# Optimization experiments

Measured on AMD Instinct MI355X. Metric: run time of the kernel, lower is better.

## Reference

```python
import jax, jax.numpy as jnp
import numpy as np

# Constant from livnium.kernel.constants (assumed scalar; value taken as 1.0).
K_O = 1.0
EPS = 1e-12  # F.normalize default eps

B, D, C = 16384, 1024, 3
F_DIM = D + 10  # features = h_final (D) + 10 scalar features


def setup_inputs() -> dict:
    key = jax.random.key(0)
    ks = jax.random.split(key, 8)
    s1 = 1.0 / np.sqrt(F_DIM)
    return {
        "h_final": jax.random.normal(ks[0], (B, D), jnp.float32),
        "v_p": jax.random.normal(ks[1], (B, D), jnp.float32),
        "v_h": jax.random.normal(ks[2], (B, D), jnp.float32),
        "neutral_dir": jax.random.normal(ks[3], (D,), jnp.float32),
        "neutral_scale": jnp.array(1.0, jnp.float32),
        "w1": jax.random.normal(ks[4], (F_DIM, F_DIM), jnp.float32) * s1,
        "b1": jnp.zeros((F_DIM,), jnp.float32),
        "w2": jax.random.normal(ks[5], (C, F_DIM), jnp.float32) * s1,
        "b2": jnp.zeros((C,), jnp.float32),
    }


def _normalize(x, axis):
    n = jnp.linalg.norm(x, axis=axis, keepdims=True)
    return x / jnp.maximum(n, EPS)


def reference(h_final, v_p, v_h, neutral_dir, neutral_scale, w1, b1, w2, b2):
    v_p_n = _normalize(v_p, -1)                      # [B, D]
    v_h_n = _normalize(v_h, -1)                      # [B, D]
    nd_n = _normalize(neutral_dir, 0)                # [D]

    # alignment(): cosine of the unit vectors == batched dot product.
    align = jnp.sum(v_p_n * v_h_n, axis=-1, keepdims=True)        # [B, 1]
    opp = jnp.sum(-v_p_n * v_h_n, axis=-1, keepdims=True)          # [B, 1]
    align_neutral_p = neutral_scale * jnp.sum(v_p_n * nd_n, axis=-1, keepdims=True)
    align_neutral_h = neutral_scale * jnp.sum(v_h_n * nd_n, axis=-1, keepdims=True)

    energy = K_O * ((1.0 + align) * 0.5)
    expose_neg = (1.0 - align) * 0.5
    dist_p_h = jnp.linalg.norm(v_h - v_p, axis=-1, keepdims=True)
    r_p = jnp.linalg.norm(v_p, axis=-1, keepdims=True)
    r_h = jnp.linalg.norm(v_h, axis=-1, keepdims=True)
    r_final = jnp.linalg.norm(h_final, axis=-1, keepdims=True)

    features = jnp.concatenate(
        [h_final, align, opp, energy, expose_neg, dist_p_h,
         r_p, r_h, r_final, align_neutral_p, align_neutral_h], axis=-1)  # [B, D+10]

    hidden = jax.nn.relu(features @ w1.T + b1)
    logits = hidden @ w2.T + b2                      # [B, C]
    return logits
```

## Files before the change

### kernel.cpp

```cpp
#include <hip/hip_runtime.h>
#include <cstdint>
#include <cstddef>

#define B_ROWS 16384
#define D_DIM  1024
#define F_REAL 1034
#define N_PAD  1152
#define K_PAD  1088
#define NKT    34
#define EPSN   1e-12f

typedef __bf16 bf16x8 __attribute__((ext_vector_type(8)));
typedef float  f32x4  __attribute__((ext_vector_type(4)));
typedef unsigned short u16;

__device__ __forceinline__ u16 f2bf(float f) {
    __bf16 b = (__bf16)f;
    return __builtin_bit_cast(u16, b);
}

__global__ __launch_bounds__(256)
void prep_kernel(const float* __restrict__ h, const float* __restrict__ vp,
                 const float* __restrict__ vh, const float* __restrict__ nd,
                 const float* __restrict__ nsp, u16* __restrict__ A)
{
    const int tid  = threadIdx.x;
    const int lane = tid & 63;
    const int wg   = blockIdx.x * 4 + (tid >> 6);
    const int r0   = wg * 4;

    const float4* ndp = (const float4*)nd;
    float4 n[4];
    #pragma unroll
    for (int c = 0; c < 4; ++c) n[c] = ndp[lane + c * 64];
    const float ns = nsp[0];

    float s_nn = 0.f;
    #pragma unroll
    for (int c = 0; c < 4; ++c)
        s_nn += n[c].x*n[c].x + n[c].y*n[c].y + n[c].z*n[c].z + n[c].w*n[c].w;
    #pragma unroll
    for (int m = 32; m >= 1; m >>= 1) s_nn += __shfl_xor(s_nn, m, 64);
    const float nnc = fmaxf(sqrtf(s_nn), EPSN);

    float4 P[2][4], Q[2][4], F[2][4];

#define LOADR(st, r)                                                          \
    do {                                                                      \
        const float4* vpp = (const float4*)(vp + (size_t)(r) * D_DIM);        \
        const float4* vhp = (const float4*)(vh + (size_t)(r) * D_DIM);        \
        const float4* hp  = (const float4*)(h  + (size_t)(r) * D_DIM);        \
        _Pragma("unroll")                                                     \
        for (int c = 0; c < 4; ++c) P[st][c] = vpp[lane + c * 64];            \
        _Pragma("unroll")                                                     \
        for (int c = 0; c < 4; ++c) Q[st][c] = vhp[lane + c * 64];            \
        _Pragma("unroll")                                                     \
        for (int c = 0; c < 4; ++c) F[st][c] = hp[lane + c * 64];             \
    } while (0)

    LOADR(0, r0);
    #pragma unroll
    for (int i = 0; i < 4; ++i) {
        const int st = i & 1;
        if (i + 1 < 4) LOADR(((i + 1) & 1), r0 + i + 1);
        __builtin_amdgcn_sched_barrier(0);

        float s_pp = 0.f, s_hh = 0.f, s_pv = 0.f, s_ff = 0.f;
        float s_dd = 0.f, s_pn = 0.f, s_hn = 0.f;
        #pragma unroll
        for (int c = 0; c < 4; ++c) {
            float4 p = P[st][c], q = Q[st][c], f = F[st][c], nn = n[c];
            s_pp += p.x*p.x + p.y*p.y + p.z*p.z + p.w*p.w;
            s_hh += q.x*q.x + q.y*q.y + q.z*q.z + q.w*q.w;
            s_pv += p.x*q.x + p.y*q.y + p.z*q.z + p.w*q.w;
            s_ff += f.x*f.x + f.y*f.y + f.z*f.z + f.w*f.w;
            float dx = q.x-p.x, dy = q.y-p.y, dz = q.z-p.z, dw = q.w-p.w;
            s_dd += dx*dx + dy*dy + dz*dz + dw*dw;
            s_pn += p.x*nn.x + p.y*nn.y + p.z*nn.z + p.w*nn.w;
            s_hn += q.x*nn.x + q.y*nn.y + q.z*nn.z + q.w*nn.w;
        }

        u16* arow = A + (size_t)(r0 + i) * K_PAD;
        #pragma unroll
        for (int c = 0; c < 4; ++c) {
            ushort4 hc;
            hc.x = f2bf(F[st][c].x); hc.y = f2bf(F[st][c].y);
            hc.z = f2bf(F[st][c].z); hc.w = f2bf(F[st][c].w);
            *(ushort4*)(arow + (lane + c * 64) * 4) = hc;
        }

        #pragma unroll
        for (int m = 32; m >= 1; m >>= 1) {
            s_pp += __shfl_xor(s_pp, m, 64);
            s_hh += __shfl_xor(s_hh, m, 64);
            s_pv += __shfl_xor(s_pv, m, 64);
            s_ff += __shfl_xor(s_ff, m, 64);
            s_dd += __shfl_xor(s_dd, m, 64);
            s_pn += __shfl_xor(s_pn, m, 64);
            s_hn += __shfl_xor(s_hn, m, 64);
        }

        if (lane == 0) {
            float np_ = sqrtf(s_pp), nh_ = sqrtf(s_hh), nf = sqrtf(s_ff);
            float npc = fmaxf(np_, EPSN), nhc = fmaxf(nh_, EPSN);
            float align = s_pv / (npc * nhc);
            u16 fo[64];
            fo[0] = f2bf(align);
            fo[1] = f2bf(-align);
            fo[2] = f2bf(0.5f * (1.0f + align));
            fo[3] = f2bf(0.5f * (1.0f - align));
            fo[4] = f2bf(sqrtf(s_dd));
            fo[5] = f2bf(np_);
            fo[6] = f2bf(nh_);
            fo[7] = f2bf(nf);
            fo[8] = f2bf(ns * s_pn / (npc * nnc));
            fo[9] = f2bf(ns * s_hn / (nhc * nnc));
            #pragma unroll
            for (int k = 10; k < 64; ++k) fo[k] = 0;
            #pragma unroll
            for (int k = 0; k < 8; ++k)
                *(uint4*)(arow + D_DIM + k * 8) = *(uint4*)(fo + k * 8);
        }
    }
#undef LOADR
}

__global__ __launch_bounds__(256)
void convw_kernel(const float* __restrict__ w1, u16* __restrict__ Bm)
{
    const int i = blockIdx.x;
    for (int j = threadIdx.x; j < K_PAD; j += 256) {
        float v = (i < F_REAL && j < F_REAL) ? w1[(size_t)i * F_REAL + j] : 0.0f;
        Bm[(size_t)i * K_PAD + j] = f2bf(v);
    }
}

__global__ __launch_bounds__(256)
void initout_kernel(const float* __restrict__ b2, float* __restrict__ out)
{
    int i = blockIdx.x * 256 + threadIdx.x;
    if (i < B_ROWS * 3) out[i] = b2[i % 3];
}

__global__ __launch_bounds__(256)
void gemm_kernel(const u16* __restrict__ A,
                 const u16* __restrict__ Bm,
                 const float* __restrict__ b1, const float* __restrict__ w2,
                 float* __restrict__ out)
{
    __shared__ __bf16 As[2 * 128 * 32];
    __shared__ __bf16 Bs[2 * 128 * 32];

    const int tid  = threadIdx.x;
    const int lane = tid & 63;
    const int wave = tid >> 6;
    const int wm = wave >> 1, wn = wave & 1;
    const int bm = blockIdx.x, bn = blockIdx.y;

    const u16* srcA[2];
    const u16* srcB[2];
    #pragma unroll
    for (int l = 0; l < 2; ++l) {
        int s   = l * 256 + tid;
        int row = s >> 2;
        int c   = (s & 3) ^ ((s >> 3) & 3);
        srcA[l] = A  + (size_t)(bm * 128 + row) * K_PAD + c * 8;
        srcB[l] = Bm + (size_t)(bn * 128 + row) * K_PAD + c * 8;
    }
    const int ldsbase = wave * 512;

#define STAGE(buf, kt)                                                        \
    do {                                                                      \
        _Pragma("unroll")                                                     \
        for (int l = 0; l < 2; ++l) {                                         \
            __builtin_amdgcn_global_load_lds(                                 \
                (const __attribute__((address_space(1))) void*)(srcA[l] + (kt) * 32), \
                (__attribute__((address_space(3))) void*)(As + (buf) * 4096 + l * 2048 + ldsbase), \
                16, 0, 0);                                                    \
            __builtin_amdgcn_global_load_lds(                                 \
                (const __attribute__((address_space(1))) void*)(srcB[l] + (kt) * 32), \
                (__attribute__((address_space(3))) void*)(Bs + (buf) * 4096 + l * 2048 + ldsbase), \
                16, 0, 0);                                                    \
        }                                                                     \
    } while (0)

    const int col  = lane & 15;
    const int quad = lane >> 4;
    const int swz  = quad ^ ((col >> 1) & 3);
    int aoff[4], boff[4];
    #pragma unroll
    for (int i = 0; i < 4; ++i)
        aoff[i] = (wm * 64 + i * 16 + col) * 32 + swz * 8;
    #pragma unroll
    for (int j = 0; j < 4; ++j)
        boff[j] = (wn * 64 + j * 16 + col) * 32 + swz * 8;

    f32x4 acc[4][4];
    #pragma unroll
    for (int i = 0; i < 4; ++i)
        #pragma unroll
        for (int j = 0; j < 4; ++j)
            acc[i][j] = (f32x4){0.f, 0.f, 0.f, 0.f};

#define COMPUTE(buf)                                                          \
    do {                                                                      \
        const __bf16* Ab = As + (buf) * 4096;                                 \
        const __bf16* Bb = Bs + (buf) * 4096;                                 \
        bf16x8 av[4], bv[4];                                                  \
        _Pragma("unroll")                                                     \
        for (int i = 0; i < 4; ++i) av[i] = *(const bf16x8*)(Ab + aoff[i]);   \
        _Pragma("unroll")                                                     \
        for (int j = 0; j < 4; ++j) bv[j] = *(const bf16x8*)(Bb + boff[j]);   \
        _Pragma("unroll")                                                     \
        for (int i = 0; i < 4; ++i)                                           \
            _Pragma("unroll")                                                 \
            for (int j = 0; j < 4; ++j)                                       \
                acc[i][j] = __builtin_amdgcn_mfma_f32_16x16x32_bf16(          \
                                av[i], bv[j], acc[i][j], 0, 0, 0);            \
    } while (0)

    STAGE(0, 0);
    __syncthreads();

    for (int kt = 0; kt < NKT; kt += 2) {
        STAGE(1, kt + 1);
        COMPUTE(0);
        __syncthreads();
        if (kt + 2 < NKT) STAGE(0, kt + 2);
        COMPUTE(1);
        __syncthreads();
    }

    float bias[4], w20[4], w21[4], w22[4];
    #pragma unroll
    for (int ni = 0; ni < 4; ++ni) {
        int n = bn * 128 + wn * 64 + ni * 16 + col;
        bool v = n < F_REAL;
        bias[ni] = v ? b1[n] : 0.0f;
        w20[ni]  = v ? w2[n] : 0.0f;
        w21[ni]  = v ? w2[F_REAL + n] : 0.0f;
        w22[ni]  = v ? w2[2 * F_REAL + n] : 0.0f;
    }
    #pragma unroll
    for (int mi = 0; mi < 4; ++mi) {
        float c0[4] = {0,0,0,0}, c1[4] = {0,0,0,0}, c2[4] = {0,0,0,0};
        #pragma unroll
        for (int ni = 0; ni < 4; ++ni) {
            #pragma unroll
            for (int r = 0; r < 4; ++r) {
                float hd = fmaxf(acc[mi][ni][r] + bias[ni], 0.0f);
                c0[r] += hd * w20[ni];
                c1[r] += hd * w21[ni];
                c2[r] += hd * w22[ni];
            }
        }
        #pragma unroll
        for (int m = 8; m >= 1; m >>= 1) {
            #pragma unroll
            for (int r = 0; r < 4; ++r) {
                c0[r] += __shfl_xor(c0[r], m, 64);
                c1[r] += __shfl_xor(c1[r], m, 64);
                c2[r] += __shfl_xor(c2[r], m, 64);
            }
        }
        if (col == 0) {
            int gm = bm * 128 + wm * 64 + mi * 16 + quad * 4;
            #pragma unroll
            for (int r = 0; r < 4; ++r) {
                atomicAdd(out + (size_t)(gm + r) * 3 + 0, c0[r]);
                atomicAdd(out + (size_t)(gm + r) * 3 + 1, c1[r]);
                atomicAdd(out + (size_t)(gm + r) * 3 + 2, c2[r]);
            }
        }
    }
#undef STAGE
#undef COMPUTE
}

extern "C" void kernel_launch(void* const* d_in, const int* in_sizes, int n_in,
                              void* d_out, int out_size, void* d_ws, size_t ws_size,
                              hipStream_t stream)
{
    const float* h  = (const float*)d_in[0];
    const float* vp = (const float*)d_in[1];
    const float* vh = (const float*)d_in[2];
    const float* nd = (const float*)d_in[3];
    const float* ns = (const float*)d_in[4];
    const float* w1 = (const float*)d_in[5];
    const float* b1 = (const float*)d_in[6];
    const float* w2 = (const float*)d_in[7];
    const float* b2 = (const float*)d_in[8];
    float* out = (float*)d_out;

    u16* Afull = (u16*)d_ws;
    u16* Bfull = Afull + (size_t)B_ROWS * K_PAD;

    prep_kernel<<<1024, 256, 0, stream>>>(h, vp, vh, nd, ns, Afull);
    convw_kernel<<<N_PAD, 256, 0, stream>>>(w1, Bfull);
    initout_kernel<<<(B_ROWS * 3 + 255) / 256, 256, 0, stream>>>(b2, out);
    gemm_kernel<<<dim3(B_ROWS / 128, N_PAD / 128), 256, 0, stream>>>(
        Afull, Bfull, b1, w2, out);
}
```

Measured before the change: 311.4 us.

## Triple-buffer GEMM K-loop with single barrier and XCD-aware block mapping

Moves the GEMM main loop from a double buffer with two barriers per iteration to a three-stage LDS ring, where each step waits only on older loads (vmcnt) and issues one barrier. The epilogue's bias and w2 loads are hoisted ahead of the loop, and MFMA sections are raised with s_setprio. The 2D grid is flattened and remapped so each XCD works on a contiguous band of row tiles across all column tiles, to improve L2 reuse of A. LDS use grows by half, and the hand-written waitcnt counts must match the loads each STAGE issues.

```diff
diff --git a/kernel.cpp b/kernel.cpp
--- a/kernel.cpp
+++ b/kernel.cpp
@@ -148,14 +148,19 @@
                  const float* __restrict__ b1, const float* __restrict__ w2,
                  float* __restrict__ out)
 {
-    __shared__ __bf16 As[2 * 128 * 32];
-    __shared__ __bf16 Bs[2 * 128 * 32];
+    __shared__ __bf16 As[3 * 128 * 32];
+    __shared__ __bf16 Bs[3 * 128 * 32];
 
     const int tid  = threadIdx.x;
     const int lane = tid & 63;
     const int wave = tid >> 6;
     const int wm = wave >> 1, wn = wave & 1;
-    const int bm = blockIdx.x, bn = blockIdx.y;
+
+    const int flat = blockIdx.x;
+    const int xcd  = flat & 7;
+    const int kk   = flat >> 3;
+    const int bm   = xcd * 16 + kk / 9;
+    const int bn   = kk % 9;
 
     const u16* srcA[2];
     const u16* srcB[2];
@@ -219,18 +224,6 @@
                                 av[i], bv[j], acc[i][j], 0, 0, 0);            \
     } while (0)
 
-    STAGE(0, 0);
-    __syncthreads();
-
-    for (int kt = 0; kt < NKT; kt += 2) {
-        STAGE(1, kt + 1);
-        COMPUTE(0);
-        __syncthreads();
-        if (kt + 2 < NKT) STAGE(0, kt + 2);
-        COMPUTE(1);
-        __syncthreads();
-    }
-
     float bias[4], w20[4], w21[4], w22[4];
     #pragma unroll
     for (int ni = 0; ni < 4; ++ni) {
@@ -241,6 +234,31 @@
         w21[ni]  = v ? w2[F_REAL + n] : 0.0f;
         w22[ni]  = v ? w2[2 * F_REAL + n] : 0.0f;
     }
+    asm volatile("s_waitcnt vmcnt(0)" ::: "memory");
+    __builtin_amdgcn_sched_barrier(0);
+
+    STAGE(0, 0);
+    STAGE(1, 1);
+
+    int cb = 0;
+    for (int t = 0; t < NKT - 1; ++t) {
+        asm volatile("s_waitcnt vmcnt(4)\n\ts_barrier" ::: "memory");
+        __builtin_amdgcn_sched_barrier(0);
+        if (t + 2 < NKT) {
+            int nb = cb + 2; if (nb >= 3) nb -= 3;
+            STAGE(nb, t + 2);
+        }
+        __builtin_amdgcn_s_setprio(1);
+        COMPUTE(cb);
+        __builtin_amdgcn_s_setprio(0);
+        if (++cb == 3) cb = 0;
+    }
+    asm volatile("s_waitcnt vmcnt(0)\n\ts_barrier" ::: "memory");
+    __builtin_amdgcn_sched_barrier(0);
+    __builtin_amdgcn_s_setprio(1);
+    COMPUTE(cb);
+    __builtin_amdgcn_s_setprio(0);
+
     #pragma unroll
     for (int mi = 0; mi < 4; ++mi) {
         float c0[4] = {0,0,0,0}, c1[4] = {0,0,0,0}, c2[4] = {0,0,0,0};
@@ -298,6 +316,6 @@
     prep_kernel<<<1024, 256, 0, stream>>>(h, vp, vh, nd, ns, Afull);
     convw_kernel<<<N_PAD, 256, 0, stream>>>(w1, Bfull);
     initout_kernel<<<(B_ROWS * 3 + 255) / 256, 256, 0, stream>>>(b2, out);
-    gemm_kernel<<<dim3(B_ROWS / 128, N_PAD / 128), 256, 0, stream>>>(
+    gemm_kernel<<<B_ROWS / 128 * (N_PAD / 128), 256, 0, stream>>>(
         Afull, Bfull, b1, w2, out);
 }
```

Result: slower. 331.7 us (+6.5%).

## Fuse h_final bf16 conversion into GEMM with LDS-resident A panel and pre-swizzled W1

Applied to the files above, without the earlier changes.

Drops the materialised bf16 A matrix. Each GEMM block of 64 rows now loads its h_final rows directly into a swizzled LDS panel, computes the row norm there, and loops over all N tiles. Each wave reads W1 straight from global memory in an MFMA fragment layout pre-arranged by convw. The scalar features go through a small side buffer. The cross-block atomics and the init kernel are replaced by an in-block reduction and a direct store, at the cost of one block per CU with large LDS and only 256 blocks.

```diff
diff --git a/kernel.cpp b/kernel.cpp
--- a/kernel.cpp
+++ b/kernel.cpp
@@ -5,14 +5,19 @@
 #define B_ROWS 16384
 #define D_DIM  1024
 #define F_REAL 1034
-#define N_PAD  1152
-#define K_PAD  1088
-#define NKT    34
+#define N2     1280
+#define NBLK   80
+#define K2     1056
+#define KT_N   33
 #define EPSN   1e-12f
+
+#define LDS_RF_OFF   65536
+#define LDS_TOTAL    134400
 
 typedef __bf16 bf16x8 __attribute__((ext_vector_type(8)));
 typedef float  f32x4  __attribute__((ext_vector_type(4)));
 typedef unsigned short u16;
+typedef unsigned int   u32;
 
 __device__ __forceinline__ u16 f2bf(float f) {
     __bf16 b = (__bf16)f;
@@ -20,9 +25,9 @@
 }
 
 __global__ __launch_bounds__(256)
-void prep_kernel(const float* __restrict__ h, const float* __restrict__ vp,
+void prep_kernel(const float* __restrict__ vp,
                  const float* __restrict__ vh, const float* __restrict__ nd,
-                 const float* __restrict__ nsp, u16* __restrict__ A)
+                 const float* __restrict__ nsp, u16* __restrict__ Ascal)
 {
     const int tid  = threadIdx.x;
     const int lane = tid & 63;
@@ -43,19 +48,16 @@
     for (int m = 32; m >= 1; m >>= 1) s_nn += __shfl_xor(s_nn, m, 64);
     const float nnc = fmaxf(sqrtf(s_nn), EPSN);
 
-    float4 P[2][4], Q[2][4], F[2][4];
+    float4 P[2][4], Q[2][4];
 
 #define LOADR(st, r)                                                          \
     do {                                                                      \
         const float4* vpp = (const float4*)(vp + (size_t)(r) * D_DIM);        \
         const float4* vhp = (const float4*)(vh + (size_t)(r) * D_DIM);        \
-        const float4* hp  = (const float4*)(h  + (size_t)(r) * D_DIM);        \
         _Pragma("unroll")                                                     \
         for (int c = 0; c < 4; ++c) P[st][c] = vpp[lane + c * 64];            \
         _Pragma("unroll")                                                     \
         for (int c = 0; c < 4; ++c) Q[st][c] = vhp[lane + c * 64];            \
-        _Pragma("unroll")                                                     \
-        for (int c = 0; c < 4; ++c) F[st][c] = hp[lane + c * 64];             \
     } while (0)
 
     LOADR(0, r0);
@@ -65,46 +67,35 @@
         if (i + 1 < 4) LOADR(((i + 1) & 1), r0 + i + 1);
         __builtin_amdgcn_sched_barrier(0);
 
-        float s_pp = 0.f, s_hh = 0.f, s_pv = 0.f, s_ff = 0.f;
+        float s_pp = 0.f, s_hh = 0.f, s_pv = 0.f;
         float s_dd = 0.f, s_pn = 0.f, s_hn = 0.f;
         #pragma unroll
         for (int c = 0; c < 4; ++c) {
-            float4 p = P[st][c], q = Q[st][c], f = F[st][c], nn = n[c];
+            float4 p = P[st][c], q = Q[st][c], nn = n[c];
             s_pp += p.x*p.x + p.y*p.y + p.z*p.z + p.w*p.w;
             s_hh += q.x*q.x + q.y*q.y + q.z*q.z + q.w*q.w;
             s_pv += p.x*q.x + p.y*q.y + p.z*q.z + p.w*q.w;
-            s_ff += f.x*f.x + f.y*f.y + f.z*f.z + f.w*f.w;
             float dx = q.x-p.x, dy = q.y-p.y, dz = q.z-p.z, dw = q.w-p.w;
             s_dd += dx*dx + dy*dy + dz*dz + dw*dw;
             s_pn += p.x*nn.x + p.y*nn.y + p.z*nn.z + p.w*nn.w;
             s_hn += q.x*nn.x + q.y*nn.y + q.z*nn.z + q.w*nn.w;
         }
 
-        u16* arow = A + (size_t)(r0 + i) * K_PAD;
-        #pragma unroll
-        for (int c = 0; c < 4; ++c) {
-            ushort4 hc;
-            hc.x = f2bf(F[st][c].x); hc.y = f2bf(F[st][c].y);
-            hc.z = f2bf(F[st][c].z); hc.w = f2bf(F[st][c].w);
-            *(ushort4*)(arow + (lane + c * 64) * 4) = hc;
-        }
-
         #pragma unroll
         for (int m = 32; m >= 1; m >>= 1) {
             s_pp += __shfl_xor(s_pp, m, 64);
             s_hh += __shfl_xor(s_hh, m, 64);
             s_pv += __shfl_xor(s_pv, m, 64);
-            s_ff += __shfl_xor(s_ff, m, 64);
             s_dd += __shfl_xor(s_dd, m, 64);
             s_pn += __shfl_xor(s_pn, m, 64);
             s_hn += __shfl_xor(s_hn, m, 64);
         }
 
         if (lane == 0) {
-            float np_ = sqrtf(s_pp), nh_ = sqrtf(s_hh), nf = sqrtf(s_ff);
+            float np_ = sqrtf(s_pp), nh_ = sqrtf(s_hh);
             float npc = fmaxf(np_, EPSN), nhc = fmaxf(nh_, EPSN);
             float align = s_pv / (npc * nhc);
-            u16 fo[64];
+            u16 fo[32];
             fo[0] = f2bf(align);
             fo[1] = f2bf(-align);
             fo[2] = f2bf(0.5f * (1.0f + align));
@@ -112,169 +103,248 @@
             fo[4] = f2bf(sqrtf(s_dd));
             fo[5] = f2bf(np_);
             fo[6] = f2bf(nh_);
-            fo[7] = f2bf(nf);
+            fo[7] = 0;
             fo[8] = f2bf(ns * s_pn / (npc * nnc));
             fo[9] = f2bf(ns * s_hn / (nhc * nnc));
             #pragma unroll
-            for (int k = 10; k < 64; ++k) fo[k] = 0;
-            #pragma unroll
-            for (int k = 0; k < 8; ++k)
-                *(uint4*)(arow + D_DIM + k * 8) = *(uint4*)(fo + k * 8);
+            for (int k = 10; k < 32; ++k) fo[k] = 0;
+            u16* arow = Ascal + (size_t)(r0 + i) * 32;
+            #pragma unroll
+            for (int k = 0; k < 4; ++k)
+                *(uint4*)(arow + k * 8) = *(uint4*)(fo + k * 8);
         }
     }
 #undef LOADR
 }
 
 __global__ __launch_bounds__(256)
-void convw_kernel(const float* __restrict__ w1, u16* __restrict__ Bm)
+void convw_kernel(const float* __restrict__ w1, u16* __restrict__ Bm2)
 {
-    const int i = blockIdx.x;
-    for (int j = threadIdx.x; j < K_PAD; j += 256) {
-        float v = (i < F_REAL && j < F_REAL) ? w1[(size_t)i * F_REAL + j] : 0.0f;
-        Bm[(size_t)i * K_PAD + j] = f2bf(v);
-    }
-}
-
-__global__ __launch_bounds__(256)
-void initout_kernel(const float* __restrict__ b2, float* __restrict__ out)
-{
-    int i = blockIdx.x * 256 + threadIdx.x;
-    if (i < B_ROWS * 3) out[i] = b2[i % 3];
-}
-
-__global__ __launch_bounds__(256)
-void gemm_kernel(const u16* __restrict__ A,
-                 const u16* __restrict__ Bm,
-                 const float* __restrict__ b1, const float* __restrict__ w2,
+    const int o = blockIdx.x * 256 + threadIdx.x;
+    const int col  = o & 15;
+    int t = o >> 4;
+    const int quad = t & 3;
+    t >>= 2;
+    const int nblk = t % NBLK;
+    const int kt   = t / NBLK;
+    const int n = nblk * 16 + col;
+    const int k = kt * 32 + quad * 8;
+
+    u16 v[8];
+    if (n < F_REAL && k + 7 < F_REAL) {
+        const float* src = w1 + (size_t)n * F_REAL + k;
+        #pragma unroll
+        for (int e = 0; e < 8; e += 2) {
+            float2 f = *(const float2*)(src + e);
+            v[e]   = f2bf(f.x);
+            v[e+1] = f2bf(f.y);
+        }
+    } else {
+        #pragma unroll
+        for (int e = 0; e < 8; ++e) {
+            float f = (n < F_REAL && k + e < F_REAL)
+                        ? w1[(size_t)n * F_REAL + k + e] : 0.0f;
+            v[e] = f2bf(f);
+        }
+    }
+    *(uint4*)(Bm2 + (size_t)o * 8) = *(uint4*)v;
+}
+
+__global__ __launch_bounds__(256, 1)
+void gemm_kernel(const float* __restrict__ h, const u16* __restrict__ Ascal,
+                 const u16* __restrict__ Bm2, const float* __restrict__ b1,
+                 const float* __restrict__ w2, const float* __restrict__ b2,
                  float* __restrict__ out)
 {
-    __shared__ __bf16 As[2 * 128 * 32];
-    __shared__ __bf16 Bs[2 * 128 * 32];
+    extern __shared__ u16 smem[];
+    u16*   panel = smem;
+    float* rf    = (float*)(smem + LDS_RF_OFF);
+    float* comb  = rf + 64;
 
     const int tid  = threadIdx.x;
     const int lane = tid & 63;
-    const int wave = tid >> 6;
-    const int wm = wave >> 1, wn = wave & 1;
-    const int bm = blockIdx.x, bn = blockIdx.y;
-
-    const u16* srcA[2];
-    const u16* srcB[2];
-    #pragma unroll
-    for (int l = 0; l < 2; ++l) {
-        int s   = l * 256 + tid;
-        int row = s >> 2;
-        int c   = (s & 3) ^ ((s >> 3) & 3);
-        srcA[l] = A  + (size_t)(bm * 128 + row) * K_PAD + c * 8;
-        srcB[l] = Bm + (size_t)(bn * 128 + row) * K_PAD + c * 8;
-    }
-    const int ldsbase = wave * 512;
-
-#define STAGE(buf, kt)                                                        \
-    do {                                                                      \
-        _Pragma("unroll")                                                     \
-        for (int l = 0; l < 2; ++l) {                                         \
-            __builtin_amdgcn_global_load_lds(                                 \
-                (const __attribute__((address_space(1))) void*)(srcA[l] + (kt) * 32), \
-                (__attribute__((address_space(3))) void*)(As + (buf) * 4096 + l * 2048 + ldsbase), \
-                16, 0, 0);                                                    \
-            __builtin_amdgcn_global_load_lds(                                 \
-                (const __attribute__((address_space(1))) void*)(srcB[l] + (kt) * 32), \
-                (__attribute__((address_space(3))) void*)(Bs + (buf) * 4096 + l * 2048 + ldsbase), \
-                16, 0, 0);                                                    \
-        }                                                                     \
-    } while (0)
-
+    const int wv   = tid >> 6;
     const int col  = lane & 15;
     const int quad = lane >> 4;
-    const int swz  = quad ^ ((col >> 1) & 3);
-    int aoff[4], boff[4];
-    #pragma unroll
-    for (int i = 0; i < 4; ++i)
-        aoff[i] = (wm * 64 + i * 16 + col) * 32 + swz * 8;
-    #pragma unroll
-    for (int j = 0; j < 4; ++j)
-        boff[j] = (wn * 64 + j * 16 + col) * 32 + swz * 8;
-
-    f32x4 acc[4][4];
-    #pragma unroll
-    for (int i = 0; i < 4; ++i)
-        #pragma unroll
-        for (int j = 0; j < 4; ++j)
-            acc[i][j] = (f32x4){0.f, 0.f, 0.f, 0.f};
-
-#define COMPUTE(buf)                                                          \
+    const int bm   = blockIdx.x;
+
+    {
+        const float* hblk = h + (size_t)bm * 64 * D_DIM;
+        const int halfsel = tid & 1;
+        const int chunkid = tid >> 1;
+        #pragma unroll 2
+        for (int jb = 0; jb < 8; ++jb) {
+            float4 v[8];
+            #pragma unroll
+            for (int u = 0; u < 8; ++u)
+                v[u] = *(const float4*)(hblk + (size_t)(jb*8+u)*D_DIM + tid*4);
+            #pragma unroll
+            for (int u = 0; u < 8; ++u) {
+                const int j = jb*8 + u;
+                ushort4 o;
+                o.x = f2bf(v[u].x); o.y = f2bf(v[u].y);
+                o.z = f2bf(v[u].z); o.w = f2bf(v[u].w);
+                *(ushort4*)(panel + j*1024 + ((chunkid ^ (j&7))*8) + halfsel*4) = o;
+            }
+        }
+    }
+    __syncthreads();
+
+    {
+        const int r = wv*16 + (lane >> 2);
+        const int q = lane & 3;
+        float ssq = 0.f;
+        #pragma unroll
+        for (int c = 0; c < 32; ++c) {
+            const int cc = q*32 + ((c + (lane >> 2)) & 31);
+            uint4 tch = *(const uint4*)(panel + r*1024 + cc*8);
+            u32 wd[4] = {tch.x, tch.y, tch.z, tch.w};
+            #pragma unroll
+            for (int e = 0; e < 4; ++e) {
+                float lo = __uint_as_float(wd[e] << 16);
+                float hi = __uint_as_float(wd[e] & 0xFFFF0000u);
+                ssq += lo*lo + hi*hi;
+            }
+        }
+        ssq += __shfl_xor(ssq, 1, 64);
+        ssq += __shfl_xor(ssq, 2, 64);
+        if (q == 0) rf[r] = sqrtf(ssq);
+    }
+    __syncthreads();
+
+    u16 rfb[4];
+    #pragma unroll
+    for (int i = 0; i < 4; ++i) rfb[i] = f2bf(rf[i*16 + col]);
+
+    const int xmask = col & 7;
+    int arow[4];
+    #pragma unroll
+    for (int i = 0; i < 4; ++i) arow[i] = (i*16 + col) * 1024;
+
+    float cacc[3][4][4];
+    #pragma unroll
+    for (int cls = 0; cls < 3; ++cls)
+        #pragma unroll
+        for (int mi = 0; mi < 4; ++mi)
+            #pragma unroll
+            for (int r = 0; r < 4; ++r) cacc[cls][mi][r] = 0.f;
+
+    for (int bnp = 0; bnp < 5; ++bnp) {
+        const int nblk0 = bnp*16 + wv*4;
+        float bias[4], w20[4], w21[4], w22[4];
+        #pragma unroll
+        for (int ni = 0; ni < 4; ++ni) {
+            const int n = (nblk0 + ni)*16 + col;
+            const bool vok = n < F_REAL;
+            bias[ni] = vok ? b1[n] : 0.f;
+            w20[ni]  = vok ? w2[n] : 0.f;
+            w21[ni]  = vok ? w2[F_REAL + n] : 0.f;
+            w22[ni]  = vok ? w2[2*F_REAL + n] : 0.f;
+        }
+        f32x4 acc[4][4];
+        #pragma unroll
+        for (int i = 0; i < 4; ++i)
+            #pragma unroll
+            for (int j = 0; j < 4; ++j)
+                acc[i][j] = (f32x4){0.f, 0.f, 0.f, 0.f};
+
+        uint4 avA[4], bvA[4], avB[4], bvB[4], avC[4], bvC[4];
+
+#define LOADF(AV, BV, kt, TAIL)                                               \
     do {                                                                      \
-        const __bf16* Ab = As + (buf) * 4096;                                 \
-        const __bf16* Bb = Bs + (buf) * 4096;                                 \
-        bf16x8 av[4], bv[4];                                                  \
-        _Pragma("unroll")                                                     \
-        for (int i = 0; i < 4; ++i) av[i] = *(const bf16x8*)(Ab + aoff[i]);   \
-        _Pragma("unroll")                                                     \
-        for (int j = 0; j < 4; ++j) bv[j] = *(const bf16x8*)(Bb + boff[j]);   \
+        if (TAIL) {                                                           \
+            _Pragma("unroll")                                                 \
+            for (int i = 0; i < 4; ++i)                                       \
+                AV[i] = *(const uint4*)(Ascal +                               \
+                         (size_t)(bm*64 + i*16 + col)*32 + quad*8);           \
+        } else {                                                              \
+            _Pragma("unroll")                                                 \
+            for (int i = 0; i < 4; ++i)                                       \
+                AV[i] = *(const uint4*)(panel + arow[i] +                     \
+                         ((((kt)*4 + quad) ^ xmask) * 8));                    \
+        }                                                                     \
+        _Pragma("unroll")                                                     \
+        for (int j = 0; j < 4; ++j)                                           \
+            BV[j] = *(const uint4*)(Bm2 +                                     \
+                     ((size_t)((kt)*NBLK + nblk0 + j)*64 + lane)*8);          \
+    } while (0)
+
+#define COMPUTE(AV, BV, TAIL)                                                 \
+    do {                                                                      \
+        bf16x8 a[4], b[4];                                                    \
+        _Pragma("unroll")                                                     \
+        for (int i = 0; i < 4; ++i) {                                         \
+            a[i] = __builtin_bit_cast(bf16x8, AV[i]);                         \
+            if (TAIL) { if (quad == 0)                                        \
+                a[i][7] = __builtin_bit_cast(__bf16, rfb[i]); }               \
+        }                                                                     \
+        _Pragma("unroll")                                                     \
+        for (int j = 0; j < 4; ++j)                                           \
+            b[j] = __builtin_bit_cast(bf16x8, BV[j]);                         \
         _Pragma("unroll")                                                     \
         for (int i = 0; i < 4; ++i)                                           \
             _Pragma("unroll")                                                 \
             for (int j = 0; j < 4; ++j)                                       \
                 acc[i][j] = __builtin_amdgcn_mfma_f32_16x16x32_bf16(          \
-                                av[i], bv[j], acc[i][j], 0, 0, 0);            \
+                                a[i], b[j], acc[i][j], 0, 0, 0);              \
     } while (0)
 
-    STAGE(0, 0);
+        LOADF(avA, bvA, 0, 0);
+        LOADF(avB, bvB, 1, 0);
+        for (int it = 0; it < 10; ++it) {
+            const int k0 = it * 3;
+            LOADF(avC, bvC, k0+2, 0);  COMPUTE(avA, bvA, 0);
+            LOADF(avA, bvA, k0+3, 0);  COMPUTE(avB, bvB, 0);
+            LOADF(avB, bvB, k0+4, 0);  COMPUTE(avC, bvC, 0);
+        }
+        LOADF(avC, bvC, 32, 1);  COMPUTE(avA, bvA, 0);
+        COMPUTE(avB, bvB, 0);
+        COMPUTE(avC, bvC, 1);
+
+        #pragma unroll
+        for (int mi = 0; mi < 4; ++mi)
+            #pragma unroll
+            for (int ni = 0; ni < 4; ++ni)
+                #pragma unroll
+                for (int r = 0; r < 4; ++r) {
+                    float hd = fmaxf(acc[mi][ni][r] + bias[ni], 0.f);
+                    cacc[0][mi][r] += hd * w20[ni];
+                    cacc[1][mi][r] += hd * w21[ni];
+                    cacc[2][mi][r] += hd * w22[ni];
+                }
+#undef LOADF
+#undef COMPUTE
+    }
+
+    #pragma unroll
+    for (int cls = 0; cls < 3; ++cls)
+        #pragma unroll
+        for (int mi = 0; mi < 4; ++mi)
+            #pragma unroll
+            for (int r = 0; r < 4; ++r) {
+                float v = cacc[cls][mi][r];
+                v += __shfl_xor(v, 8, 64);
+                v += __shfl_xor(v, 4, 64);
+                v += __shfl_xor(v, 2, 64);
+                v += __shfl_xor(v, 1, 64);
+                cacc[cls][mi][r] = v;
+            }
+
+    if (col == 0) {
+        #pragma unroll
+        for (int cls = 0; cls < 3; ++cls)
+            #pragma unroll
+            for (int mi = 0; mi < 4; ++mi)
+                #pragma unroll
+                for (int r = 0; r < 4; ++r)
+                    comb[wv*192 + (mi*16 + quad*4 + r)*3 + cls] = cacc[cls][mi][r];
+    }
     __syncthreads();
-
-    for (int kt = 0; kt < NKT; kt += 2) {
-        STAGE(1, kt + 1);
-        COMPUTE(0);
-        __syncthreads();
-        if (kt + 2 < NKT) STAGE(0, kt + 2);
-        COMPUTE(1);
-        __syncthreads();
-    }
-
-    float bias[4], w20[4], w21[4], w22[4];
-    #pragma unroll
-    for (int ni = 0; ni < 4; ++ni) {
-        int n = bn * 128 + wn * 64 + ni * 16 + col;
-        bool v = n < F_REAL;
-        bias[ni] = v ? b1[n] : 0.0f;
-        w20[ni]  = v ? w2[n] : 0.0f;
-        w21[ni]  = v ? w2[F_REAL + n] : 0.0f;
-        w22[ni]  = v ? w2[2 * F_REAL + n] : 0.0f;
-    }
-    #pragma unroll
-    for (int mi = 0; mi < 4; ++mi) {
-        float c0[4] = {0,0,0,0}, c1[4] = {0,0,0,0}, c2[4] = {0,0,0,0};
-        #pragma unroll
-        for (int ni = 0; ni < 4; ++ni) {
-            #pragma unroll
-            for (int r = 0; r < 4; ++r) {
-                float hd = fmaxf(acc[mi][ni][r] + bias[ni], 0.0f);
-                c0[r] += hd * w20[ni];
-                c1[r] += hd * w21[ni];
-                c2[r] += hd * w22[ni];
-            }
-        }
-        #pragma unroll
-        for (int m = 8; m >= 1; m >>= 1) {
-            #pragma unroll
-            for (int r = 0; r < 4; ++r) {
-                c0[r] += __shfl_xor(c0[r], m, 64);
-                c1[r] += __shfl_xor(c1[r], m, 64);
-                c2[r] += __shfl_xor(c2[r], m, 64);
-            }
-        }
-        if (col == 0) {
-            int gm = bm * 128 + wm * 64 + mi * 16 + quad * 4;
-            #pragma unroll
-            for (int r = 0; r < 4; ++r) {
-                atomicAdd(out + (size_t)(gm + r) * 3 + 0, c0[r]);
-                atomicAdd(out + (size_t)(gm + r) * 3 + 1, c1[r]);
-                atomicAdd(out + (size_t)(gm + r) * 3 + 2, c2[r]);
-            }
-        }
-    }
-#undef STAGE
-#undef COMPUTE
+    if (tid < 192) {
+        float s = comb[tid] + comb[192+tid] + comb[384+tid] + comb[576+tid]
+                + b2[tid % 3];
+        out[(size_t)bm * 192 + tid] = s;
+    }
 }
 
 extern "C" void kernel_launch(void* const* d_in, const int* in_sizes, int n_in,
@@ -292,12 +362,18 @@
     const float* b2 = (const float*)d_in[8];
     float* out = (float*)d_out;
 
-    u16* Afull = (u16*)d_ws;
-    u16* Bfull = Afull + (size_t)B_ROWS * K_PAD;
-
-    prep_kernel<<<1024, 256, 0, stream>>>(h, vp, vh, nd, ns, Afull);
-    convw_kernel<<<N_PAD, 256, 0, stream>>>(w1, Bfull);
-    initout_kernel<<<(B_ROWS * 3 + 255) / 256, 256, 0, stream>>>(b2, out);
-    gemm_kernel<<<dim3(B_ROWS / 128, N_PAD / 128), 256, 0, stream>>>(
-        Afull, Bfull, b1, w2, out);
-}
+    u16* Ascal = (u16*)d_ws;
+    u16* Bm2   = Ascal + (size_t)B_ROWS * 32;
+
+    static bool attr_done = false;
+    if (!attr_done) {
+        (void)hipFuncSetAttribute((const void*)gemm_kernel,
+                                  hipFuncAttributeMaxDynamicSharedMemorySize,
+                                  LDS_TOTAL);
+        attr_done = true;
+    }
+
+    prep_kernel<<<1024, 256, 0, stream>>>(vp, vh, nd, ns, Ascal);
+    convw_kernel<<<660, 256, 0, stream>>>(w1, Bm2);
+    gemm_kernel<<<256, 256, LDS_TOTAL, stream>>>(h, Ascal, Bm2, b1, w2, b2, out);
+}
```

New measurement: 267.7 us. -14.0%, faster.
